# Kernel optimization log

Measured on AMD Instinct MI355X. Metric: run time of the kernel, lower is better.

The kernel has to match this reference:

```python
import jax, jax.numpy as jnp
import numpy as np

BN_EPS = 1e-5

def _bn(x, g, b, m, v):
    # eval-mode BatchNorm1d with running stats
    return (x - m) * jax.lax.rsqrt(v + BN_EPS) * g + b

def _gcn(h, src, dst, norm, W, b, N):
    # PyG GCNConv: out[dst] += norm * (h @ W)[src]; then add bias
    msg = (h @ W)[src] * norm[:, None]
    return jax.ops.segment_sum(msg, dst, num_segments=N) + b

def setup_inputs() -> dict:
    key = jax.random.key(0)
    ks = jax.random.split(key, 24)
    N, E, F = 300000, 3000000, 25
    d = {}
    d['x'] = jax.random.normal(ks[0], (N, F), jnp.float32)
    d['edge_index'] = jax.random.randint(ks[1], (2, E), 0, N, dtype=jnp.int64)
    def lin(k, i, o):
        return jax.random.normal(k, (i, o), jnp.float32) / np.float32(np.sqrt(i))
    # ffn1: Linear(25,100) -> BN(100) -> ReLU -> Dropout -> Linear(100,25) -> BN(25) -> Dropout
    d['W1'] = lin(ks[2], 25, 100); d['b1'] = jnp.zeros((100,), jnp.float32)
    d['g1'] = jnp.ones((100,), jnp.float32); d['beta1'] = jnp.zeros((100,), jnp.float32)
    d['m1'] = jnp.zeros((100,), jnp.float32); d['v1'] = jnp.ones((100,), jnp.float32)
    d['W2'] = lin(ks[3], 100, 25); d['b2'] = jnp.zeros((25,), jnp.float32)
    d['g2'] = jnp.ones((25,), jnp.float32); d['beta2'] = jnp.zeros((25,), jnp.float32)
    d['m2'] = jnp.zeros((25,), jnp.float32); d['v2'] = jnp.ones((25,), jnp.float32)
    # GCN layers actually used in forward
    d['Wc1'] = lin(ks[4], 25, 25); d['bc1'] = jnp.zeros((25,), jnp.float32)
    d['Wc2'] = lin(ks[5], 25, 16); d['bc2'] = jnp.zeros((16,), jnp.float32)
    d['Wc3'] = lin(ks[6], 16, 16); d['bc3'] = jnp.zeros((16,), jnp.float32)
    d['Wc4'] = lin(ks[7], 16, 8);  d['bc4'] = jnp.zeros((8,), jnp.float32)
    d['Wc5'] = lin(ks[8], 8, 4);   d['bc5'] = jnp.zeros((4,), jnp.float32)
    # fc: reshape yields 1200 cols (source's Linear(4800,4) is a bug; use 1200)
    d['Wfc'] = lin(ks[9], 1200, 4); d['bfc'] = jnp.zeros((4,), jnp.float32)
    return d

def reference(x, edge_index, W1, b1, g1, beta1, m1, v1, W2, b2, g2, beta2, m2, v2,
              Wc1, bc1, Wc2, bc2, Wc3, bc3, Wc4, bc4, Wc5, bc5, Wfc, bfc):
    N = x.shape[0]
    # add self-loops and compute symmetric normalization once (shared graph)
    loops = jnp.arange(N, dtype=edge_index.dtype)
    src = jnp.concatenate([edge_index[0], loops])
    dst = jnp.concatenate([edge_index[1], loops])
    deg = jax.ops.segment_sum(jnp.ones_like(dst, jnp.float32), dst, num_segments=N)
    dinv = jnp.where(deg > 0, jax.lax.rsqrt(deg), 0.0)
    norm = dinv[src] * dinv[dst]
    # ffn1 (eval mode: dropout is identity)
    h = _bn(x @ W1 + b1, g1, beta1, m1, v1)
    h = jax.nn.relu(h)
    h = _bn(h @ W2 + b2, g2, beta2, m2, v2)
    # stacked GCN layers
    h = jax.nn.relu(_gcn(h, src, dst, norm, Wc1, bc1, N))
    h = jax.nn.relu(_gcn(h, src, dst, norm, Wc2, bc2, N))
    h = jax.nn.relu(_gcn(h, src, dst, norm, Wc3, bc3, N))
    h = jax.nn.relu(_gcn(h, src, dst, norm, Wc4, bc4, N))
    h = jax.nn.relu(_gcn(h, src, dst, norm, Wc5, bc5, N))
    h = h.reshape(-1, 300 * 4)  # [N/300, 1200]
    return h @ Wfc + bfc
```

## Files before the change

kernel.cpp:

```cpp
#include <hip/hip_runtime.h>

#define BN_EPS 1e-5f
#define ELLW 48
#define BSH2 11
#define NPB 2048
#define MAXBK 160
#define BCAP2 26624

struct PartS {
    int hist[MAXBK];
    int cur[MAXBK];
    int gbase[MAXBK];
    int locstart[MAXBK + 1];
    int sc[256];
    int stage[1024];
};

__global__ __launch_bounds__(256) void k_setup(
    const float* __restrict__ W1, const float* __restrict__ b1,
    const float* __restrict__ g1, const float* __restrict__ be1,
    const float* __restrict__ m1, const float* __restrict__ v1,
    const float* __restrict__ W2, const float* __restrict__ b2,
    const float* __restrict__ g2, const float* __restrict__ be2,
    const float* __restrict__ m2, const float* __restrict__ v2,
    const float* __restrict__ Wc1, float* __restrict__ prep,
    const unsigned int* __restrict__ ei2, int* __restrict__ flag,
    int* __restrict__ gcnt)
{
    int t = threadIdx.x;
    if (blockIdx.x == 1) {
        if (t < MAXBK) gcnt[t] = 0;
        if (t < 64) {
            unsigned int v = ei2[2 * t + 1];
            unsigned long long mask = __ballot(v != 0);
            if (t == 0) flag[0] = (mask == 0ULL) ? 1 : 0;
        }
        return;
    }
    __shared__ float s1[100], bb1[100], s2[25], bb2[25], wc[625];
    if (t < 100) {
        float s = g1[t] * rsqrtf(v1[t] + BN_EPS);
        s1[t] = s; bb1[t] = (b1[t] - m1[t]) * s + be1[t];
    }
    if (t >= 128 && t < 153) {
        int u = t - 128;
        float s = g2[u] * rsqrtf(v2[u] + BN_EPS);
        s2[u] = s; bb2[u] = (b2[u] - m2[u]) * s + be2[u];
    }
    for (int q = t; q < 625; q += 256) wc[q] = Wc1[q];
    __syncthreads();
    for (int q = t; q < 2500; q += 256) {
        int kc = q / 625, r = q % 625;
        int j = r / 25, kk = r % 25;
        int k = kc * 25 + kk;
        prep[q] = W1[j * 100 + k] * s1[k];
    }
    for (int q = t; q < 2500; q += 256) {
        int kc = q / 625, r = q % 625;
        int kk = r / 25, j = r % 25;
        int k = kc * 25 + kk;
        float acc = 0.0f;
        for (int m = 0; m < 25; ++m) acc += W2[k * 25 + m] * s2[m] * wc[m * 25 + j];
        prep[2500 + q] = acc;
    }
    if (t < 100) prep[5000 + t] = bb1[t];
    if (t >= 128 && t < 153) {
        int j = t - 128;
        float acc = 0.0f;
        for (int m = 0; m < 25; ++m) acc += bb2[m] * wc[m * 25 + j];
        prep[5104 + j] = acc;
    }
}

__global__ __launch_bounds__(256, 4) void k_ffnpart(
    const float* __restrict__ prep, const float* __restrict__ x,
    float* __restrict__ T,
    const int* __restrict__ ei, const int* __restrict__ flag,
    int* __restrict__ gcnt, int* __restrict__ bdata,
    int nFfn, int N, int E)
{
    __shared__ char smem_raw[sizeof(PartS)];
    int t = threadIdx.x;

    if ((int)blockIdx.x < nFfn) {
        int n = (int)blockIdx.x * 256 + t;
        if (n >= N) return;

        float xi[25];
#pragma unroll
        for (int j = 0; j < 25; ++j) xi[j] = x[(size_t)n * 25 + j];

        float o[25];
#pragma unroll
        for (int j = 0; j < 25; ++j) o[j] = 0.0f;

#pragma unroll 1
        for (int kc = 0; kc < 4; ++kc) {
            const float* __restrict__ w1c = prep + kc * 625;
            const float* __restrict__ w2c = prep + 2500 + kc * 625;
            const float* __restrict__ b1c = prep + 5000 + kc * 25;
            float hm[25];
#pragma unroll
            for (int kk = 0; kk < 25; ++kk) hm[kk] = b1c[kk];
#pragma unroll
            for (int j = 0; j < 25; ++j) {
                float xv = xi[j];
#pragma unroll
                for (int kk = 0; kk < 25; ++kk) hm[kk] += xv * w1c[j * 25 + kk];
            }
#pragma unroll
            for (int kk = 0; kk < 25; ++kk) {
                float r = fmaxf(hm[kk], 0.0f);
#pragma unroll
                for (int j = 0; j < 25; ++j) o[j] += r * w2c[kk * 25 + j];
            }
        }

        float o32[32];
#pragma unroll
        for (int j = 0; j < 25; ++j) o32[j] = o[j] + prep[5104 + j];
#pragma unroll
        for (int j = 25; j < 32; ++j) o32[j] = 0.0f;
        float4* T4 = (float4*)(T + (size_t)n * 32);
#pragma unroll
        for (int q = 0; q < 8; ++q)
            T4[q] = make_float4(o32[4 * q], o32[4 * q + 1], o32[4 * q + 2], o32[4 * q + 3]);
    } else {
        PartS& S = *reinterpret_cast<PartS*>(smem_raw);
        int blockBase = ((int)blockIdx.x - nFfn) * 1024;
        int blockCnt = E - blockBase; if (blockCnt > 1024) blockCnt = 1024; if (blockCnt < 0) blockCnt = 0;

        for (int i = t; i < MAXBK; i += 256) S.hist[i] = 0;
        __syncthreads();

        bool w64 = (flag[0] != 0);
        int e = blockBase + t * 4;
        int s[4], d[4];
        int cnt = 0;
        if (e < E) {
            cnt = E - e; if (cnt > 4) cnt = 4;
            if (cnt == 4) {
                if (w64) {
                    const int4* ps = (const int4*)(ei + (size_t)2 * e);
                    int4 a = ps[0], b = ps[1];
                    s[0] = a.x; s[1] = a.z; s[2] = b.x; s[3] = b.z;
                    const int4* pd = (const int4*)(ei + (size_t)2 * ((size_t)E + e));
                    int4 c = pd[0], f = pd[1];
                    d[0] = c.x; d[1] = c.z; d[2] = f.x; d[3] = f.z;
                } else {
                    int4 a = *(const int4*)(ei + e);
                    s[0] = a.x; s[1] = a.y; s[2] = a.z; s[3] = a.w;
                    int4 c = *(const int4*)(ei + (size_t)E + e);
                    d[0] = c.x; d[1] = c.y; d[2] = c.z; d[3] = c.w;
                }
            } else {
                for (int i = 0; i < cnt; ++i) {
                    if (w64) { s[i] = ei[(size_t)2 * (e + i)]; d[i] = ei[(size_t)2 * ((size_t)E + e + i)]; }
                    else     { s[i] = ei[e + i];               d[i] = ei[(size_t)E + e + i]; }
                }
            }
        }
        int bk[4], pk[4];
        for (int i = 0; i < cnt; ++i) {
            bk[i] = d[i] >> BSH2;
            pk[i] = (s[i] << BSH2) | (d[i] & (NPB - 1));
            atomicAdd(&S.hist[bk[i]], 1);
        }
        __syncthreads();

        S.sc[t] = (t < MAXBK) ? S.hist[t] : 0;
        __syncthreads();
        for (int off = 1; off < 256; off <<= 1) {
            int xv = (t >= off) ? S.sc[t - off] : 0;
            __syncthreads();
            S.sc[t] += xv;
            __syncthreads();
        }
        if (t < MAXBK) {
            S.locstart[t] = S.sc[t] - S.hist[t];
            S.cur[t] = S.sc[t] - S.hist[t];
            if (S.hist[t] > 0) S.gbase[t] = atomicAdd(&gcnt[t], S.hist[t]);
        }
        if (t == 255) S.locstart[MAXBK] = S.sc[MAXBK - 1];
        __syncthreads();

        for (int i = 0; i < cnt; ++i) {
            int p = atomicAdd(&S.cur[bk[i]], 1);
            S.stage[p] = pk[i];
        }
        __syncthreads();

        for (int sIdx = t; sIdx < blockCnt; sIdx += 256) {
            int lo = 0, hi = MAXBK;
            while (hi - lo > 1) {
                int mid = (lo + hi) >> 1;
                if (S.locstart[mid] <= sIdx) lo = mid; else hi = mid;
            }
            int gp = S.gbase[lo] + (sIdx - S.locstart[lo]);
            if (gp < BCAP2) bdata[(size_t)lo * BCAP2 + gp] = S.stage[sIdx];
        }
    }
}

__global__ __launch_bounds__(256) void k_ell2(
    const int* __restrict__ gcnt, const int* __restrict__ bdata,
    int* __restrict__ ell, float* __restrict__ dinv, int N)
{
    __shared__ int lcnt[NPB];
    int b = blockIdx.x;
    int t = threadIdx.x;
    for (int i = t; i < NPB; i += 256) lcnt[i] = 0;
    __syncthreads();
    int base = b << BSH2;
    int cnt = min(gcnt[b], BCAP2);
    const int* __restrict__ bd = bdata + (size_t)b * BCAP2;
    for (int i = t; i < cnt; i += 256) {
        int v = bd[i];
        int dl = v & (NPB - 1);
        int src = v >> BSH2;
        int pos = atomicAdd(&lcnt[dl], 1);
        if (pos < ELLW - 4)
            ell[(size_t)(base + dl) * ELLW + 4 + pos] = src;
    }
    __syncthreads();
    for (int i = t; i < NPB; i += 256) {
        int n = base + i;
        if (n < N) {
            int c = lcnt[i];
            ell[(size_t)n * ELLW] = c;
            dinv[n] = 1.0f / sqrtf((float)(c + 1));
        }
    }
}

template <int DI, int SI, int DO, int LPN, bool SDV>
__global__ __launch_bounds__(256) void k_layer(
    const int* __restrict__ ell,
    const float* __restrict__ dinv, const float* __restrict__ bias,
    const float* __restrict__ W,
    const float* __restrict__ Tin, float* __restrict__ Tout, int N)
{
    constexpr int SI4 = SI / 4;
    constexpr int DO4 = DO / 4;
    constexpr int PAD = LPN * 4;
    __shared__ float sW[DI * DO];
    __shared__ float sB[PAD];
    int t = threadIdx.x;
    for (int i = t; i < DI * DO; i += 256) sW[i] = W[i];
    for (int i = t; i < PAD; i += 256) sB[i] = (i < DI) ? bias[i] : 0.0f;
    __syncthreads();

    int g = t / LPN;
    int j = t % LPN;
    int n = blockIdx.x * (256 / LPN) + g;
    int nc = (n < N) ? n : (N - 1);
    const int* __restrict__ row = ell + (size_t)nc * ELLW;
    int dg = min(row[0], ELLW - 4);
    if (n >= N) dg = 0;
    if (4 * j >= DI) dg = 0;
    float dv = dinv[nc];
    const float4* __restrict__ T4 = (const float4*)Tin;

    float4 a0 = T4[(size_t)nc * SI4 + j];
    if (SDV) { a0.x *= dv; a0.y *= dv; a0.z *= dv; a0.w *= dv; }
    float4 a1 = make_float4(0.f, 0.f, 0.f, 0.f);
    float4 a2 = a1, a3 = a1;
    const int4* __restrict__ rowv = (const int4*)(row + 4);
    int k = 0;
    int4 s4;
    if (k + 3 < dg) s4 = rowv[0];
    for (; k + 3 < dg; k += 4) {
        bool more = (k + 7 < dg);
        int4 nx;
        if (more) nx = rowv[(k >> 2) + 1];
        float4 v0 = T4[(size_t)s4.x * SI4 + j];
        float4 v1 = T4[(size_t)s4.y * SI4 + j];
        float4 v2 = T4[(size_t)s4.z * SI4 + j];
        float4 v3 = T4[(size_t)s4.w * SI4 + j];
        if (SDV) {
            float d0 = dinv[s4.x], d1 = dinv[s4.y], d2 = dinv[s4.z], d3 = dinv[s4.w];
            a0.x += d0 * v0.x; a0.y += d0 * v0.y; a0.z += d0 * v0.z; a0.w += d0 * v0.w;
            a1.x += d1 * v1.x; a1.y += d1 * v1.y; a1.z += d1 * v1.z; a1.w += d1 * v1.w;
            a2.x += d2 * v2.x; a2.y += d2 * v2.y; a2.z += d2 * v2.z; a2.w += d2 * v2.w;
            a3.x += d3 * v3.x; a3.y += d3 * v3.y; a3.z += d3 * v3.z; a3.w += d3 * v3.w;
        } else {
            a0.x += v0.x; a0.y += v0.y; a0.z += v0.z; a0.w += v0.w;
            a1.x += v1.x; a1.y += v1.y; a1.z += v1.z; a1.w += v1.w;
            a2.x += v2.x; a2.y += v2.y; a2.z += v2.z; a2.w += v2.w;
            a3.x += v3.x; a3.y += v3.y; a3.z += v3.z; a3.w += v3.w;
        }
        if (more) s4 = nx;
    }
    for (; k < dg; ++k) {
        int sidx = row[4 + k];
        float4 v = T4[(size_t)sidx * SI4 + j];
        float dd = SDV ? dinv[sidx] : 1.0f;
        a0.x += dd * v.x; a0.y += dd * v.y; a0.z += dd * v.z; a0.w += dd * v.w;
    }
    float ar[4];
    ar[0] = fmaxf(dv * (a0.x + a1.x + a2.x + a3.x) + sB[4 * j + 0], 0.0f);
    ar[1] = fmaxf(dv * (a0.y + a1.y + a2.y + a3.y) + sB[4 * j + 1], 0.0f);
    ar[2] = fmaxf(dv * (a0.z + a1.z + a2.z + a3.z) + sB[4 * j + 2], 0.0f);
    ar[3] = fmaxf(dv * (a0.w + a1.w + a2.w + a3.w) + sB[4 * j + 3], 0.0f);

    int lane = t & 63;
    int base = lane - j;
    int jo = (j < DO4) ? j : 0;
    const float4* __restrict__ sW4 = (const float4*)sW;
    float4 o = make_float4(0.f, 0.f, 0.f, 0.f);
#pragma unroll
    for (int k2 = 0; k2 < DI; ++k2) {
        float av = __shfl(ar[k2 & 3], base + (k2 >> 2));
        float4 w = sW4[k2 * DO4 + jo];
        o.x += av * w.x; o.y += av * w.y; o.z += av * w.z; o.w += av * w.w;
    }
    if (n < N && j < DO4)
        ((float4*)Tout)[(size_t)n * DO4 + j] =
            make_float4(dv * o.x, dv * o.y, dv * o.z, dv * o.w);
}

__global__ __launch_bounds__(256) void k_fc(
    const int* __restrict__ ell, const float* __restrict__ dinv,
    const float* __restrict__ bc5,
    const float* __restrict__ Tin,
    const float* __restrict__ Wfc, const float* __restrict__ bfc,
    float* __restrict__ out, int N)
{
    __shared__ float sH[300 * 4];
    int r = blockIdx.x;
    int t = threadIdx.x;
    int base300 = r * 300;
    const float4* __restrict__ T4 = (const float4*)Tin;
    float4 b5 = *(const float4*)bc5;

    for (int i = t; i < 300; i += 256) {
        int n = base300 + i;
        float4 a0 = make_float4(0.f, 0.f, 0.f, 0.f);
        float4 a1 = a0, a2 = a0, a3 = a0;
        float dv = 0.0f;
        if (n < N) {
            const int* __restrict__ row = ell + (size_t)n * ELLW;
            int dg = min(row[0], ELLW - 4);
            dv = dinv[n];
            a0 = T4[n];
            const int4* __restrict__ rowv = (const int4*)(row + 4);
            int k = 0;
            for (; k + 3 < dg; k += 4) {
                int4 s4 = rowv[k >> 2];
                float4 v0 = T4[s4.x], v1 = T4[s4.y], v2 = T4[s4.z], v3 = T4[s4.w];
                a0.x += v0.x; a0.y += v0.y; a0.z += v0.z; a0.w += v0.w;
                a1.x += v1.x; a1.y += v1.y; a1.z += v1.z; a1.w += v1.w;
                a2.x += v2.x; a2.y += v2.y; a2.z += v2.z; a2.w += v2.w;
                a3.x += v3.x; a3.y += v3.y; a3.z += v3.z; a3.w += v3.w;
            }
            for (; k < dg; ++k) {
                float4 v = T4[row[4 + k]];
                a0.x += v.x; a0.y += v.y; a0.z += v.z; a0.w += v.w;
            }
        }
        ((float4*)sH)[i] = make_float4(
            fmaxf(dv * (a0.x + a1.x + a2.x + a3.x) + b5.x, 0.0f),
            fmaxf(dv * (a0.y + a1.y + a2.y + a3.y) + b5.y, 0.0f),
            fmaxf(dv * (a0.z + a1.z + a2.z + a3.z) + b5.z, 0.0f),
            fmaxf(dv * (a0.w + a1.w + a2.w + a3.w) + b5.w, 0.0f));
    }
    __syncthreads();

    float p0 = 0.f, p1 = 0.f, p2 = 0.f, p3 = 0.f;
    for (int k = t; k < 1200; k += 256) {
        float h = sH[k];
        p0 += h * Wfc[k * 4 + 0];
        p1 += h * Wfc[k * 4 + 1];
        p2 += h * Wfc[k * 4 + 2];
        p3 += h * Wfc[k * 4 + 3];
    }
#pragma unroll
    for (int off2 = 32; off2 > 0; off2 >>= 1) {
        p0 += __shfl_down(p0, off2);
        p1 += __shfl_down(p1, off2);
        p2 += __shfl_down(p2, off2);
        p3 += __shfl_down(p3, off2);
    }
    __shared__ float red[4][4];
    int w = t >> 6, lane = t & 63;
    if (lane == 0) { red[w][0] = p0; red[w][1] = p1; red[w][2] = p2; red[w][3] = p3; }
    __syncthreads();
    if (t < 4) {
        float s = red[0][t] + red[1][t] + red[2][t] + red[3][t];
        out[r * 4 + t] = s + bfc[t];
    }
}

extern "C" void kernel_launch(void* const* d_in, const int* in_sizes, int n_in,
                              void* d_out, int out_size, void* d_ws, size_t ws_size,
                              hipStream_t stream) {
    const float* x   = (const float*)d_in[0];
    const int*   ei  = (const int*)d_in[1];
    const float* W1  = (const float*)d_in[2];
    const float* b1  = (const float*)d_in[3];
    const float* g1  = (const float*)d_in[4];
    const float* be1 = (const float*)d_in[5];
    const float* m1  = (const float*)d_in[6];
    const float* v1  = (const float*)d_in[7];
    const float* W2  = (const float*)d_in[8];
    const float* b2  = (const float*)d_in[9];
    const float* g2  = (const float*)d_in[10];
    const float* be2 = (const float*)d_in[11];
    const float* m2  = (const float*)d_in[12];
    const float* v2  = (const float*)d_in[13];
    const float* Wc1 = (const float*)d_in[14];
    const float* bc1 = (const float*)d_in[15];
    const float* Wc2 = (const float*)d_in[16];
    const float* bc2 = (const float*)d_in[17];
    const float* Wc3 = (const float*)d_in[18];
    const float* bc3 = (const float*)d_in[19];
    const float* Wc4 = (const float*)d_in[20];
    const float* bc4 = (const float*)d_in[21];
    const float* Wc5 = (const float*)d_in[22];
    const float* bc5 = (const float*)d_in[23];
    const float* Wfc = (const float*)d_in[24];
    const float* bfc = (const float*)d_in[25];

    const int N = in_sizes[0] / 25;
    const int E = in_sizes[1] / 2;
    const int NBUCK = (N + NPB - 1) >> BSH2;
    const int NROW = out_size / 4;

    char* ws = (char*)d_ws;
    size_t off = 0;
    auto alloc = [&](size_t bytes) { size_t o = off; off += (bytes + 255) & ~(size_t)255; return o; };
    size_t o_flag = alloc(256);
    size_t o_gcnt = alloc((size_t)MAXBK * 4);
    size_t o_prep = alloc(6144 * 4);
    size_t o_dinv = alloc((size_t)N * 4);
    size_t o_ell  = alloc((size_t)N * ELLW * 4);
    size_t o_A = alloc((size_t)N * 32 * 4);
    size_t o_B = alloc((size_t)N * 16 * 4);
    (void)alloc(4096);

    int*   flag = (int*)(ws + o_flag);
    int*   gcnt = (int*)(ws + o_gcnt);
    float* prep = (float*)(ws + o_prep);
    float* dinv = (float*)(ws + o_dinv);
    int*   ell  = (int*)(ws + o_ell);
    float* A = (float*)(ws + o_A);
    float* B_ = (float*)(ws + o_B);
    int*   bdata = (int*)B_;

    const int B = 256;
    int gN = (N + B - 1) / B;
    int gF = gN;
    int gP = (E + 1023) / 1024;

    k_setup<<<2, B, 0, stream>>>(W1, b1, g1, be1, m1, v1, W2, b2, g2, be2, m2, v2,
                                 Wc1, prep, (const unsigned int*)ei, flag, gcnt);
    k_ffnpart<<<gF + gP, B, 0, stream>>>(prep, x, A, ei, flag, gcnt, bdata, gF, N, E);
    k_ell2<<<NBUCK, B, 0, stream>>>(gcnt, bdata, ell, dinv, N);

    k_layer<25, 32, 16, 8, true><<<(N * 8 + B - 1) / B, B, 0, stream>>>(ell, dinv, bc1, Wc2, A, B_, N);
    k_layer<16, 16, 16, 4, false><<<(N * 4 + B - 1) / B, B, 0, stream>>>(ell, dinv, bc2, Wc3, B_, A, N);
    k_layer<16, 16, 8, 4, false><<<(N * 4 + B - 1) / B, B, 0, stream>>>(ell, dinv, bc3, Wc4, A, B_, N);
    k_layer<8, 8, 4, 2, false><<<(N * 2 + B - 1) / B, B, 0, stream>>>(ell, dinv, bc4, Wc5, B_, A, N);
    k_fc<<<NROW, B, 0, stream>>>(ell, dinv, bc5, A, Wfc, bfc, (float*)d_out, N);
}
```

Before: 474.8 us.

## Sort nodes by degree via counting-sort permutation for balanced GCN layer waves

```diff
diff --git a/kernel.cpp b/kernel.cpp
--- a/kernel.cpp
+++ b/kernel.cpp
@@ -25,11 +25,12 @@
     const float* __restrict__ m2, const float* __restrict__ v2,
     const float* __restrict__ Wc1, float* __restrict__ prep,
     const unsigned int* __restrict__ ei2, int* __restrict__ flag,
-    int* __restrict__ gcnt)
+    int* __restrict__ gcnt, int* __restrict__ ghist)
 {
     int t = threadIdx.x;
     if (blockIdx.x == 1) {
         if (t < MAXBK) gcnt[t] = 0;
+        if (t >= 192 && t < 256) ghist[t - 192] = 0;
         if (t < 64) {
             unsigned int v = ei2[2 * t + 1];
             unsigned long long mask = __ballot(v != 0);
@@ -204,12 +205,15 @@
 
 __global__ __launch_bounds__(256) void k_ell2(
     const int* __restrict__ gcnt, const int* __restrict__ bdata,
-    int* __restrict__ ell, float* __restrict__ dinv, int N)
+    int* __restrict__ ell, float* __restrict__ dinv,
+    int* __restrict__ deg, int* __restrict__ ghist, int N)
 {
     __shared__ int lcnt[NPB];
+    __shared__ int lhist[64];
     int b = blockIdx.x;
     int t = threadIdx.x;
     for (int i = t; i < NPB; i += 256) lcnt[i] = 0;
+    if (t < 64) lhist[t] = 0;
     __syncthreads();
     int base = b << BSH2;
     int cnt = min(gcnt[b], BCAP2);
@@ -228,14 +232,49 @@
         if (n < N) {
             int c = lcnt[i];
             ell[(size_t)n * ELLW] = c;
+            deg[n] = c;
             dinv[n] = 1.0f / sqrtf((float)(c + 1));
-        }
+            atomicAdd(&lhist[c < 63 ? c : 63], 1);
+        }
+    }
+    __syncthreads();
+    if (t < 64 && lhist[t] > 0) atomicAdd(&ghist[t], lhist[t]);
+}
+
+__global__ void k_off(const int* __restrict__ ghist, int* __restrict__ gcur) {
+    int t = threadIdx.x;
+    int h = ghist[t];
+    int v = h;
+    for (int off = 1; off < 64; off <<= 1) {
+        int u = __shfl_up(v, off);
+        if (t >= off) v += u;
+    }
+    gcur[t] = v - h;
+}
+
+__global__ __launch_bounds__(256) void k_perm(
+    const int* __restrict__ deg, int* __restrict__ gcur,
+    int* __restrict__ perm, int N)
+{
+    __shared__ int lh[64], lbase[64], lcur[64];
+    int t = threadIdx.x;
+    if (t < 64) { lh[t] = 0; lcur[t] = 0; }
+    __syncthreads();
+    int n = blockIdx.x * 256 + t;
+    int c = -1;
+    if (n < N) { c = deg[n]; c = (c < 63) ? c : 63; atomicAdd(&lh[c], 1); }
+    __syncthreads();
+    if (t < 64 && lh[t] > 0) lbase[t] = atomicAdd(&gcur[t], lh[t]);
+    __syncthreads();
+    if (n < N) {
+        int p = atomicAdd(&lcur[c], 1);
+        perm[lbase[c] + p] = n;
     }
 }
 
 template <int DI, int SI, int DO, int LPN, bool SDV>
 __global__ __launch_bounds__(256) void k_layer(
-    const int* __restrict__ ell,
+    const int* __restrict__ perm, const int* __restrict__ ell,
     const float* __restrict__ dinv, const float* __restrict__ bias,
     const float* __restrict__ W,
     const float* __restrict__ Tin, float* __restrict__ Tout, int N)
@@ -252,16 +291,17 @@
 
     int g = t / LPN;
     int j = t % LPN;
-    int n = blockIdx.x * (256 / LPN) + g;
-    int nc = (n < N) ? n : (N - 1);
-    const int* __restrict__ row = ell + (size_t)nc * ELLW;
+    int nlin = blockIdx.x * (256 / LPN) + g;
+    int nl = (nlin < N) ? nlin : (N - 1);
+    int nd = perm[nl];
+    const int* __restrict__ row = ell + (size_t)nd * ELLW;
     int dg = min(row[0], ELLW - 4);
-    if (n >= N) dg = 0;
+    if (nlin >= N) dg = 0;
     if (4 * j >= DI) dg = 0;
-    float dv = dinv[nc];
+    float dv = dinv[nd];
     const float4* __restrict__ T4 = (const float4*)Tin;
 
-    float4 a0 = T4[(size_t)nc * SI4 + j];
+    float4 a0 = T4[(size_t)nd * SI4 + j];
     if (SDV) { a0.x *= dv; a0.y *= dv; a0.z *= dv; a0.w *= dv; }
     float4 a1 = make_float4(0.f, 0.f, 0.f, 0.f);
     float4 a2 = a1, a3 = a1;
@@ -314,8 +354,8 @@
         float4 w = sW4[k2 * DO4 + jo];
         o.x += av * w.x; o.y += av * w.y; o.z += av * w.z; o.w += av * w.w;
     }
-    if (n < N && j < DO4)
-        ((float4*)Tout)[(size_t)n * DO4 + j] =
+    if (nlin < N && j < DO4)
+        ((float4*)Tout)[(size_t)nd * DO4 + j] =
             make_float4(dv * o.x, dv * o.y, dv * o.z, dv * o.w);
 }
 
@@ -431,8 +471,11 @@
     auto alloc = [&](size_t bytes) { size_t o = off; off += (bytes + 255) & ~(size_t)255; return o; };
     size_t o_flag = alloc(256);
     size_t o_gcnt = alloc((size_t)MAXBK * 4);
+    size_t o_hist = alloc(512);
     size_t o_prep = alloc(6144 * 4);
     size_t o_dinv = alloc((size_t)N * 4);
+    size_t o_deg  = alloc((size_t)N * 4);
+    size_t o_perm = alloc((size_t)N * 4);
     size_t o_ell  = alloc((size_t)N * ELLW * 4);
     size_t o_A = alloc((size_t)N * 32 * 4);
     size_t o_B = alloc((size_t)N * 16 * 4);
@@ -440,8 +483,12 @@
 
     int*   flag = (int*)(ws + o_flag);
     int*   gcnt = (int*)(ws + o_gcnt);
+    int*   ghist = (int*)(ws + o_hist);
+    int*   gcur  = ghist + 64;
     float* prep = (float*)(ws + o_prep);
     float* dinv = (float*)(ws + o_dinv);
+    int*   deg  = (int*)(ws + o_deg);
+    int*   perm = (int*)(ws + o_perm);
     int*   ell  = (int*)(ws + o_ell);
     float* A = (float*)(ws + o_A);
     float* B_ = (float*)(ws + o_B);
@@ -453,13 +500,15 @@
     int gP = (E + 1023) / 1024;
 
     k_setup<<<2, B, 0, stream>>>(W1, b1, g1, be1, m1, v1, W2, b2, g2, be2, m2, v2,
-                                 Wc1, prep, (const unsigned int*)ei, flag, gcnt);
+                                 Wc1, prep, (const unsigned int*)ei, flag, gcnt, ghist);
     k_ffnpart<<<gF + gP, B, 0, stream>>>(prep, x, A, ei, flag, gcnt, bdata, gF, N, E);
-    k_ell2<<<NBUCK, B, 0, stream>>>(gcnt, bdata, ell, dinv, N);
-
-    k_layer<25, 32, 16, 8, true><<<(N * 8 + B - 1) / B, B, 0, stream>>>(ell, dinv, bc1, Wc2, A, B_, N);
-    k_layer<16, 16, 16, 4, false><<<(N * 4 + B - 1) / B, B, 0, stream>>>(ell, dinv, bc2, Wc3, B_, A, N);
-    k_layer<16, 16, 8, 4, false><<<(N * 4 + B - 1) / B, B, 0, stream>>>(ell, dinv, bc3, Wc4, A, B_, N);
-    k_layer<8, 8, 4, 2, false><<<(N * 2 + B - 1) / B, B, 0, stream>>>(ell, dinv, bc4, Wc5, B_, A, N);
+    k_ell2<<<NBUCK, B, 0, stream>>>(gcnt, bdata, ell, dinv, deg, ghist, N);
+    k_off<<<1, 64, 0, stream>>>(ghist, gcur);
+    k_perm<<<gN, B, 0, stream>>>(deg, gcur, perm, N);
+
+    k_layer<25, 32, 16, 8, true><<<(N * 8 + B - 1) / B, B, 0, stream>>>(perm, ell, dinv, bc1, Wc2, A, B_, N);
+    k_layer<16, 16, 16, 4, false><<<(N * 4 + B - 1) / B, B, 0, stream>>>(perm, ell, dinv, bc2, Wc3, B_, A, N);
+    k_layer<16, 16, 8, 4, false><<<(N * 4 + B - 1) / B, B, 0, stream>>>(perm, ell, dinv, bc3, Wc4, A, B_, N);
+    k_layer<8, 8, 4, 2, false><<<(N * 2 + B - 1) / B, B, 0, stream>>>(perm, ell, dinv, bc4, Wc5, B_, A, N);
     k_fc<<<NROW, B, 0, stream>>>(ell, dinv, bc5, A, Wfc, bfc, (float*)d_out, N);
 }
```

Measured after the change: 517.8 us. 9.0% more time.
